# Kernel optimization log

Hardware: AMD Instinct MI355X
Metric: run time of the kernel (lower is better)

Reference implementation:

```python
import jax, jax.numpy as jnp
import numpy as np

# Daubechies-2 (db2) filter bank coefficients, as in pywt.Wavelet('db2')
_DEC_LO = np.array([-0.12940952255126037, 0.22414386804185735, 0.8365163037378079, 0.48296291314453416], dtype=np.float32)
_DEC_HI = np.array([-0.48296291314453416, 0.8365163037378079, -0.22414386804185735, -0.12940952255126037], dtype=np.float32)
_REC_LO = _DEC_LO[::-1].copy()
_REC_HI = _DEC_HI[::-1].copy()
_FLEN = 4


def _conv_valid(x, h):
    # np.convolve(x, h, 'valid') along last axis (true convolution: filter flipped)
    F = h.shape[0]
    N = x.shape[-1]
    hf = h[::-1]
    out = hf[0] * x[..., 0:N - F + 1]
    for k in range(1, F):
        out = out + hf[k] * x[..., k:N - F + 1 + k]
    return out


def dwt_db2(x):
    # pywt.dwt(x, 'db2') with default symmetric mode, axis=-1. x: (B, N) -> (B, (N+3)//2) x2
    xe = jnp.pad(x, ((0, 0), (_FLEN - 1, _FLEN - 1)), mode='symmetric')
    lo = jnp.asarray(_DEC_LO, dtype=x.dtype)
    hi = jnp.asarray(_DEC_HI, dtype=x.dtype)
    cA = _conv_valid(xe, lo)[..., 1::2]
    cD = _conv_valid(xe, hi)[..., 1::2]
    return cA, cD


def idwt_db2(cA, cD):
    # pywt.idwt(cA, cD, 'db2'): upsample-by-2 (len 2L-1), full conv with rec filters,
    # trim (flen-2) each side == pad by 1 and valid conv. Output length 2L - flen + 2.
    L = cA.shape[-1]
    def up(c):
        u = jnp.zeros(c.shape[:-1] + (2 * L - 1,), dtype=c.dtype)
        return u.at[..., ::2].set(c)
    uA = jnp.pad(up(cA), ((0, 0), (1, 1)))
    uD = jnp.pad(up(cD), ((0, 0), (1, 1)))
    rlo = jnp.asarray(_REC_LO, dtype=cA.dtype)
    rhi = jnp.asarray(_REC_HI, dtype=cA.dtype)
    return _conv_valid(uA, rlo) + _conv_valid(uD, rhi)


def setup_inputs() -> dict:
    key = jax.random.key(0)
    k1, k2 = jax.random.split(key)
    B, N = 4096, 4096
    output_dim = (N + 3) // 2  # 2049
    x = jax.random.normal(k1, (B, N), dtype=jnp.float32)
    # keras 'uniform' initializer: U(-0.05, 0.05), shape (input_shape[1], output_dim)
    kernel = jax.random.uniform(k2, (N, output_dim), dtype=jnp.float32, minval=-0.05, maxval=0.05)
    return {"x": x, "kernel": kernel}


def reference(x, kernel):
    cA, cD = dwt_db2(x)            # (B, L)
    cA = cA * kernel               # learned multiplicative gain
    cD = cD * kernel
    y = idwt_db2(cA, cD)           # (B, 2L - 2) == (B, N)
    return jax.nn.relu(y)
```

## Files before the change

### kernel.cpp

```cpp
#include <hip/hip_runtime.h>


#define NN 4096
#define LL 2049
#define TPR 512

typedef float v4f __attribute__((ext_vector_type(4)));

__global__ __launch_bounds__(256) void wavelet_fused(const float* __restrict__ x,
                                                     const float* __restrict__ ker,
                                                     float* __restrict__ out) {
    const int row = blockIdx.y;
    const int t   = blockIdx.x * 256 + threadIdx.x;
    const int base = 8 * t;

    const float lo0 = -0.12940952255126037f, lo1 = 0.22414386804185735f,
                lo2 =  0.8365163037378079f,  lo3 = 0.48296291314453416f;
    const float hi0 = -0.48296291314453416f, hi1 = 0.8365163037378079f,
                hi2 = -0.22414386804185735f, hi3 = -0.12940952255126037f;

    const float* xrow = x + (size_t)row * NN;
    const bool first = (t == 0);
    const bool last  = (t == TPR - 1);

    const float4 c0 = *(const float4*)(xrow + base);
    const float4 c1 = *(const float4*)(xrow + base + 4);
    const int la = first ? 0 : (base - 2);
    const int ra = last ? (NN - 2) : (base + 8);
    const float2 hl = *(const float2*)(xrow + la);
    const float2 hr = *(const float2*)(xrow + ra);

    float E[12];
    E[0] = first ? hl.y : hl.x;
    E[1] = first ? hl.x : hl.y;
    E[2] = c0.x; E[3] = c0.y; E[4] = c0.z; E[5] = c0.w;
    E[6] = c1.x; E[7] = c1.y; E[8] = c1.z; E[9] = c1.w;
    E[10] = last ? hr.y : hr.x;
    E[11] = last ? hr.x : hr.y;

    const float* krow = ker + (size_t)row * LL + 4 * t;
    float g[5];
    #pragma unroll
    for (int i = 0; i < 5; ++i) g[i] = krow[i];

    float A[5], D[5];
    #pragma unroll
    for (int i = 0; i < 5; ++i) {
        const float e0 = E[2 * i], e1 = E[2 * i + 1], e2 = E[2 * i + 2], e3 = E[2 * i + 3];
        const float cA = lo3 * e0 + lo2 * e1 + lo1 * e2 + lo0 * e3;
        const float cD = hi3 * e0 + hi2 * e1 + hi1 * e2 + hi0 * e3;
        A[i] = g[i] * cA;
        D[i] = g[i] * cD;
    }

    float y[8];
    #pragma unroll
    for (int i = 0; i < 4; ++i) {
        float ye = lo1 * A[i] + lo3 * A[i + 1] + hi1 * D[i] + hi3 * D[i + 1];
        float yo = lo0 * A[i] + lo2 * A[i + 1] + hi0 * D[i] + hi2 * D[i + 1];
        y[2 * i]     = fmaxf(ye, 0.0f);
        y[2 * i + 1] = fmaxf(yo, 0.0f);
    }

    float* orow = out + (size_t)row * NN + base;
    v4f w0 = { y[0], y[1], y[2], y[3] };
    v4f w1 = { y[4], y[5], y[6], y[7] };
    __builtin_nontemporal_store(w0, (v4f*)orow);
    __builtin_nontemporal_store(w1, (v4f*)(orow + 4));
}

extern "C" void kernel_launch(void* const* d_in, const int* in_sizes, int n_in,
                              void* d_out, int out_size, void* d_ws, size_t ws_size,
                              hipStream_t stream) {
    const float* x   = (const float*)d_in[0];
    const float* ker = (const float*)d_in[1];
    float* out = (float*)d_out;
    wavelet_fused<<<dim3(TPR / 256, 4096), dim3(256), 0, stream>>>(x, ker, out);
}
```

Measured before the change: 142.7 us.

## Process two rows per thread and switch to regular stores

Each thread now handles the same column slice for two adjacent rows, with all loads for both rows issued up front. The grid's row dimension is halved to match. This raises memory-level parallelism per thread and halves the block count. The output stores are changed from nontemporal to ordinary float4 stores, which changes cache behaviour on the write path.

```diff
diff --git a/kernel.cpp b/kernel.cpp
--- a/kernel.cpp
+++ b/kernel.cpp
@@ -5,13 +5,11 @@
 #define LL 2049
 #define TPR 512
 
-typedef float v4f __attribute__((ext_vector_type(4)));
-
 __global__ __launch_bounds__(256) void wavelet_fused(const float* __restrict__ x,
                                                      const float* __restrict__ ker,
                                                      float* __restrict__ out) {
-    const int row = blockIdx.y;
-    const int t   = blockIdx.x * 256 + threadIdx.x;
+    const int row0 = 2 * blockIdx.y;
+    const int t    = blockIdx.x * 256 + threadIdx.x;
     const int base = 8 * t;
 
     const float lo0 = -0.12940952255126037f, lo1 = 0.22414386804185735f,
@@ -19,54 +17,73 @@
     const float hi0 = -0.48296291314453416f, hi1 = 0.8365163037378079f,
                 hi2 = -0.22414386804185735f, hi3 = -0.12940952255126037f;
 
-    const float* xrow = x + (size_t)row * NN;
     const bool first = (t == 0);
     const bool last  = (t == TPR - 1);
-
-    const float4 c0 = *(const float4*)(xrow + base);
-    const float4 c1 = *(const float4*)(xrow + base + 4);
     const int la = first ? 0 : (base - 2);
     const int ra = last ? (NN - 2) : (base + 8);
-    const float2 hl = *(const float2*)(xrow + la);
-    const float2 hr = *(const float2*)(xrow + ra);
 
-    float E[12];
-    E[0] = first ? hl.y : hl.x;
-    E[1] = first ? hl.x : hl.y;
-    E[2] = c0.x; E[3] = c0.y; E[4] = c0.z; E[5] = c0.w;
-    E[6] = c1.x; E[7] = c1.y; E[8] = c1.z; E[9] = c1.w;
-    E[10] = last ? hr.y : hr.x;
-    E[11] = last ? hr.x : hr.y;
+    const float* xr0 = x + (size_t)row0 * NN;
+    const float* xr1 = xr0 + NN;
+    const float4 c0a = *(const float4*)(xr0 + base);
+    const float4 c1a = *(const float4*)(xr0 + base + 4);
+    const float2 hla = *(const float2*)(xr0 + la);
+    const float2 hra = *(const float2*)(xr0 + ra);
+    const float4 c0b = *(const float4*)(xr1 + base);
+    const float4 c1b = *(const float4*)(xr1 + base + 4);
+    const float2 hlb = *(const float2*)(xr1 + la);
+    const float2 hrb = *(const float2*)(xr1 + ra);
 
-    const float* krow = ker + (size_t)row * LL + 4 * t;
-    float g[5];
+    const float* kr0 = ker + (size_t)row0 * LL + 4 * t;
+    const float* kr1 = kr0 + LL;
+    float ga[5], gb[5];
     #pragma unroll
-    for (int i = 0; i < 5; ++i) g[i] = krow[i];
+    for (int i = 0; i < 5; ++i) ga[i] = kr0[i];
+    #pragma unroll
+    for (int i = 0; i < 5; ++i) gb[i] = kr1[i];
 
-    float A[5], D[5];
+    float* orow0 = out + (size_t)row0 * NN + base;
+    float* orow1 = orow0 + NN;
+
     #pragma unroll
-    for (int i = 0; i < 5; ++i) {
-        const float e0 = E[2 * i], e1 = E[2 * i + 1], e2 = E[2 * i + 2], e3 = E[2 * i + 3];
-        const float cA = lo3 * e0 + lo2 * e1 + lo1 * e2 + lo0 * e3;
-        const float cD = hi3 * e0 + hi2 * e1 + hi1 * e2 + hi0 * e3;
-        A[i] = g[i] * cA;
-        D[i] = g[i] * cD;
+    for (int r = 0; r < 2; ++r) {
+        const float4 c0 = r ? c0b : c0a;
+        const float4 c1 = r ? c1b : c1a;
+        const float2 hl = r ? hlb : hla;
+        const float2 hr = r ? hrb : hra;
+        const float* g  = r ? gb : ga;
+
+        float E[12];
+        E[0] = first ? hl.y : hl.x;
+        E[1] = first ? hl.x : hl.y;
+        E[2] = c0.x; E[3] = c0.y; E[4] = c0.z; E[5] = c0.w;
+        E[6] = c1.x; E[7] = c1.y; E[8] = c1.z; E[9] = c1.w;
+        E[10] = last ? hr.y : hr.x;
+        E[11] = last ? hr.x : hr.y;
+
+        float A[5], D[5];
+        #pragma unroll
+        for (int i = 0; i < 5; ++i) {
+            const float e0 = E[2 * i], e1 = E[2 * i + 1];
+            const float e2 = E[2 * i + 2], e3 = E[2 * i + 3];
+            const float cA = lo3 * e0 + lo2 * e1 + lo1 * e2 + lo0 * e3;
+            const float cD = hi3 * e0 + hi2 * e1 + hi1 * e2 + hi0 * e3;
+            A[i] = g[i] * cA;
+            D[i] = g[i] * cD;
+        }
+
+        float y[8];
+        #pragma unroll
+        for (int i = 0; i < 4; ++i) {
+            float ye = lo1 * A[i] + lo3 * A[i + 1] + hi1 * D[i] + hi3 * D[i + 1];
+            float yo = lo0 * A[i] + lo2 * A[i + 1] + hi0 * D[i] + hi2 * D[i + 1];
+            y[2 * i]     = fmaxf(ye, 0.0f);
+            y[2 * i + 1] = fmaxf(yo, 0.0f);
+        }
+
+        float* orow = r ? orow1 : orow0;
+        *(float4*)(orow)     = make_float4(y[0], y[1], y[2], y[3]);
+        *(float4*)(orow + 4) = make_float4(y[4], y[5], y[6], y[7]);
     }
-
-    float y[8];
-    #pragma unroll
-    for (int i = 0; i < 4; ++i) {
-        float ye = lo1 * A[i] + lo3 * A[i + 1] + hi1 * D[i] + hi3 * D[i + 1];
-        float yo = lo0 * A[i] + lo2 * A[i + 1] + hi0 * D[i] + hi2 * D[i + 1];
-        y[2 * i]     = fmaxf(ye, 0.0f);
-        y[2 * i + 1] = fmaxf(yo, 0.0f);
-    }
-
-    float* orow = out + (size_t)row * NN + base;
-    v4f w0 = { y[0], y[1], y[2], y[3] };
-    v4f w1 = { y[4], y[5], y[6], y[7] };
-    __builtin_nontemporal_store(w0, (v4f*)orow);
-    __builtin_nontemporal_store(w1, (v4f*)(orow + 4));
 }
 
 extern "C" void kernel_launch(void* const* d_in, const int* in_sizes, int n_in,
@@ -75,5 +92,5 @@
     const float* x   = (const float*)d_in[0];
     const float* ker = (const float*)d_in[1];
     float* out = (float*)d_out;
-    wavelet_fused<<<dim3(TPR / 256, 4096), dim3(256), 0, stream>>>(x, ker, out);
+    wavelet_fused<<<dim3(TPR / 256, 2048), dim3(256), 0, stream>>>(x, ker, out);
 }
```

Result: no change. 139.9 us (-1.9%).

## Use persistent grid-stride loop with software-prefetched loads

Applied to the files above, without the earlier changes.

Replaces the one-octet-per-thread grid of 8192 blocks with 2048 blocks that each iterate four times over the rows. Loads for the next iteration are issued before the current one is computed, to hide memory latency. It also swaps the nontemporal output stores for plain float4 stores, which may change how the output interacts with the cache. Fewer waves are resident per block, and the double-buffered batch raises register use.

```diff
diff --git a/kernel.cpp b/kernel.cpp
--- a/kernel.cpp
+++ b/kernel.cpp
@@ -3,50 +3,61 @@
 
 #define NN 4096
 #define LL 2049
-#define TPR 512
+#define OCTS 512
+#define NBLK 2048
+#define NTHR 256
+#define STRIDE (NBLK * NTHR)
+#define ITERS ((4096 * OCTS) / STRIDE)
 
-typedef float v4f __attribute__((ext_vector_type(4)));
+struct Batch {
+    float4 c0, c1;
+    float2 hl, hr;
+    float g0, g1, g2, g3, g4;
+};
 
-__global__ __launch_bounds__(256) void wavelet_fused(const float* __restrict__ x,
-                                                     const float* __restrict__ ker,
-                                                     float* __restrict__ out) {
-    const int row = blockIdx.y;
-    const int t   = blockIdx.x * 256 + threadIdx.x;
-    const int base = 8 * t;
+__device__ __forceinline__ void load_batch(Batch& b, const float* __restrict__ x,
+                                           const float* __restrict__ ker, int tau) {
+    const int row  = tau >> 9;
+    const int u    = tau & (OCTS - 1);
+    const int base = 8 * u;
+    const float* xrow = x + (size_t)row * NN;
+    const bool first = (u == 0);
+    const bool last  = (u == OCTS - 1);
+    const int la = first ? 0 : (base - 2);
+    const int ra = last ? (NN - 2) : (base + 8);
+    b.c0 = *(const float4*)(xrow + base);
+    b.c1 = *(const float4*)(xrow + base + 4);
+    b.hl = *(const float2*)(xrow + la);
+    b.hr = *(const float2*)(xrow + ra);
+    const float* krow = ker + (size_t)row * LL + 4 * u;
+    b.g0 = krow[0]; b.g1 = krow[1]; b.g2 = krow[2]; b.g3 = krow[3]; b.g4 = krow[4];
+}
 
+__device__ __forceinline__ void process(const Batch& b, float* __restrict__ out, int tau) {
     const float lo0 = -0.12940952255126037f, lo1 = 0.22414386804185735f,
                 lo2 =  0.8365163037378079f,  lo3 = 0.48296291314453416f;
     const float hi0 = -0.48296291314453416f, hi1 = 0.8365163037378079f,
                 hi2 = -0.22414386804185735f, hi3 = -0.12940952255126037f;
 
-    const float* xrow = x + (size_t)row * NN;
-    const bool first = (t == 0);
-    const bool last  = (t == TPR - 1);
-
-    const float4 c0 = *(const float4*)(xrow + base);
-    const float4 c1 = *(const float4*)(xrow + base + 4);
-    const int la = first ? 0 : (base - 2);
-    const int ra = last ? (NN - 2) : (base + 8);
-    const float2 hl = *(const float2*)(xrow + la);
-    const float2 hr = *(const float2*)(xrow + ra);
+    const int row  = tau >> 9;
+    const int u    = tau & (OCTS - 1);
+    const bool first = (u == 0);
+    const bool last  = (u == OCTS - 1);
 
     float E[12];
-    E[0] = first ? hl.y : hl.x;
-    E[1] = first ? hl.x : hl.y;
-    E[2] = c0.x; E[3] = c0.y; E[4] = c0.z; E[5] = c0.w;
-    E[6] = c1.x; E[7] = c1.y; E[8] = c1.z; E[9] = c1.w;
-    E[10] = last ? hr.y : hr.x;
-    E[11] = last ? hr.x : hr.y;
+    E[0] = first ? b.hl.y : b.hl.x;
+    E[1] = first ? b.hl.x : b.hl.y;
+    E[2] = b.c0.x; E[3] = b.c0.y; E[4] = b.c0.z; E[5] = b.c0.w;
+    E[6] = b.c1.x; E[7] = b.c1.y; E[8] = b.c1.z; E[9] = b.c1.w;
+    E[10] = last ? b.hr.y : b.hr.x;
+    E[11] = last ? b.hr.x : b.hr.y;
 
-    const float* krow = ker + (size_t)row * LL + 4 * t;
-    float g[5];
-    #pragma unroll
-    for (int i = 0; i < 5; ++i) g[i] = krow[i];
-
+    const float g[5] = { b.g0, b.g1, b.g2, b.g3, b.g4 };
     float A[5], D[5];
     #pragma unroll
     for (int i = 0; i < 5; ++i) {
-        const float e0 = E[2 * i], e1 = E[2 * i + 1], e2 = E[2 * i + 2], e3 = E[2 * i + 3];
+        const float e0 = E[2 * i], e1 = E[2 * i + 1];
+        const float e2 = E[2 * i + 2], e3 = E[2 * i + 3];
         const float cA = lo3 * e0 + lo2 * e1 + lo1 * e2 + lo0 * e3;
         const float cD = hi3 * e0 + hi2 * e1 + hi1 * e2 + hi0 * e3;
         A[i] = g[i] * cA;
@@ -62,11 +73,24 @@
         y[2 * i + 1] = fmaxf(yo, 0.0f);
     }
 
-    float* orow = out + (size_t)row * NN + base;
-    v4f w0 = { y[0], y[1], y[2], y[3] };
-    v4f w1 = { y[4], y[5], y[6], y[7] };
-    __builtin_nontemporal_store(w0, (v4f*)orow);
-    __builtin_nontemporal_store(w1, (v4f*)(orow + 4));
+    float* orow = out + (size_t)row * NN + 8 * u;
+    *(float4*)(orow)     = make_float4(y[0], y[1], y[2], y[3]);
+    *(float4*)(orow + 4) = make_float4(y[4], y[5], y[6], y[7]);
+}
+
+__global__ __launch_bounds__(NTHR) void wavelet_fused(const float* __restrict__ x,
+                                                      const float* __restrict__ ker,
+                                                      float* __restrict__ out) {
+    const int tid = blockIdx.x * NTHR + threadIdx.x;
+
+    Batch cur, nxt;
+    load_batch(cur, x, ker, tid);
+    #pragma unroll
+    for (int k = 0; k < ITERS; ++k) {
+        if (k + 1 < ITERS) load_batch(nxt, x, ker, tid + (k + 1) * STRIDE);
+        process(cur, out, tid + k * STRIDE);
+        cur = nxt;
+    }
 }
 
 extern "C" void kernel_launch(void* const* d_in, const int* in_sizes, int n_in,
@@ -75,5 +99,5 @@
     const float* x   = (const float*)d_in[0];
     const float* ker = (const float*)d_in[1];
     float* out = (float*)d_out;
-    wavelet_fused<<<dim3(TPR / 256, 4096), dim3(256), 0, stream>>>(x, ker, out);
+    wavelet_fused<<<dim3(NBLK), dim3(NTHR), 0, stream>>>(x, ker, out);
 }
```

After: 141.8 us. About the same (-0.6%).
